# Performance work log

Measured on AMD Instinct MI355X. Metric: run time of the kernel, lower is better.

The kernel has to match this reference:

```python
import jax, jax.numpy as jnp
import numpy as np
import math

N_QUBITS = 8
EMBED_DIM = 8
NUM_HEADS = 2
N_QLAYERS = 2
TWO_PI = 2.0 * math.pi


def _apply_rx(state, theta, wire):
    # state: (N,) + (2,)*n complex64; theta: scalar or (N,)
    n = state.ndim - 1
    ax = 1 + wire
    a0 = jnp.take(state, 0, axis=ax)
    a1 = jnp.take(state, 1, axis=ax)
    half = jnp.asarray(theta) * 0.5
    c = jnp.cos(half)
    s = jnp.sin(half)
    if c.ndim:  # per-sample angle -> broadcast over remaining qubit axes
        bshape = (-1,) + (1,) * (n - 1)
        c = c.reshape(bshape)
        s = s.reshape(bshape)
    js = 1j * s
    n0 = c * a0 - js * a1
    n1 = -js * a0 + c * a1
    return jnp.stack([n0, n1], axis=ax)


def _apply_cnot(state, ctrl, tgt):
    ac, at = 1 + ctrl, 1 + tgt
    s0 = jnp.take(state, 0, axis=ac)
    s1 = jnp.take(state, 1, axis=ac)
    at2 = at - 1 if at > ac else at  # target axis index after removing control axis
    s1 = jnp.flip(s1, axis=at2)
    return jnp.stack([s0, s1], axis=ac)


def qnode(inputs, weights):
    """AngleEmbedding(RX) + BasicEntanglerLayers(RX + CNOT ring), PauliZ expvals.
    inputs: (N, n) angles; weights: (L, n). Returns (N, n) expvals, fully batched."""
    N, n = inputs.shape
    L = weights.shape[0]
    state = jnp.zeros((N,) + (2,) * n, jnp.complex64)
    state = state.at[(slice(None),) + (0,) * n].set(1.0)
    for i in range(n):  # AngleEmbedding: RX(inputs[:, i]) on wire i
        state = _apply_rx(state, inputs[:, i], i)
    for l in range(L):  # BasicEntanglerLayers
        for i in range(n):
            state = _apply_rx(state, weights[l, i], i)
        for i in range(n):
            state = _apply_cnot(state, i, (i + 1) % n)
    probs = (state.real ** 2 + state.imag ** 2).reshape(N, 2 ** n)
    # wire 0 is the most significant bit of the flattened statevector index
    idx = jnp.arange(2 ** n)
    bits = (idx[:, None] >> jnp.arange(n - 1, -1, -1)[None, :]) & 1  # (2^n, n)
    signs = (1.0 - 2.0 * bits).astype(probs.dtype)
    return probs @ signs  # (N, n)


def _qproj(x, weights):
    # apply qnode to every (batch, timestep) vector at once (vectorized loop fusion)
    B, S, E = x.shape
    return qnode(x.reshape(B * S, E), weights).reshape(B, S, E)


def _attention_forward(q, k, v, wq_w, wk_w, wv_w, wd_w):
    B, S, E = q.shape
    H, D = NUM_HEADS, EMBED_DIM // NUM_HEADS
    qp = _qproj(q, wq_w)
    kp = _qproj(k, wk_w)
    vp = _qproj(v, wv_w)
    # split heads: (B, H, S, D)
    qh = qp.reshape(B, S, H, D).transpose(0, 2, 1, 3)
    kh = kp.reshape(B, S, H, D).transpose(0, 2, 1, 3)
    vh = vp.reshape(B, S, H, D).transpose(0, 2, 1, 3)
    scores = jnp.einsum('bhqd,bhkd->bhqk', qh, kh) / jnp.sqrt(jnp.asarray(D, qh.dtype))
    attn = jax.nn.softmax(scores, axis=-1)
    ctx = jnp.einsum('bhqk,bhkd->bhqd', attn, vh)
    concat = ctx.transpose(0, 2, 1, 3).reshape(B, S, E)
    out = _qproj(concat, wd_w)
    return out, attn


def setup_inputs() -> dict:
    key = jax.random.key(0)
    kq, kk, kv, k1, k2, k3, k4 = jax.random.split(key, 7)
    B, S, E = 32, 1024, EMBED_DIM
    return {
        'q': jax.random.normal(kq, (B, S, E), jnp.float32),
        'k': jax.random.normal(kk, (B, S, E), jnp.float32),
        'v': jax.random.normal(kv, (B, S, E), jnp.float32),
        'wq_weights': jax.random.uniform(k1, (N_QLAYERS, N_QUBITS), jnp.float32) * TWO_PI,
        'wk_weights': jax.random.uniform(k2, (N_QLAYERS, N_QUBITS), jnp.float32) * TWO_PI,
        'wv_weights': jax.random.uniform(k3, (N_QLAYERS, N_QUBITS), jnp.float32) * TWO_PI,
        'dense_weights': jax.random.uniform(k4, (N_QLAYERS, N_QUBITS), jnp.float32) * TWO_PI,
    }


def reference(q, k, v, wq_weights, wk_weights, wv_weights, dense_weights):
    return _attention_forward(q, k, v, wq_weights, wk_weights, wv_weights, dense_weights)
```

## Files before the change

### kernel.cpp

```cpp
#include <hip/hip_runtime.h>
#include <math.h>


#define NSAMP 32768

#define QX1 0xB1
#define QX2 0x4E
#define QX3 0x1B
#define ROW_MIRROR 0x140
#define ROW_HALF_MIRROR 0x141

template <int CTRL>
__device__ __forceinline__ float dppf(float x) {
  int xi = __float_as_int(x);
  return __int_as_float(
      __builtin_amdgcn_update_dpp(xi, xi, CTRL, 0xF, 0xF, false));
}

template <int P1>
__device__ __forceinline__ float dpp2x(float x) {
  return dppf<ROW_HALF_MIRROR>(dppf<P1>(x));
}


template <int CTRL>
__device__ __forceinline__ void cg1(float c, float s, float* vr, float* vi) {
#pragma unroll
  for (int m = 0; m < 32; ++m) {
    const float pr = dppf<CTRL>(vr[m]);
    const float pi = dppf<CTRL>(vi[m]);
    vr[m] = fmaf(c, vr[m], s * pi);
    vi[m] = fmaf(c, vi[m], -s * pr);
  }
}

template <int P1>
__device__ __forceinline__ void cg2(float c, float s, float* vr, float* vi) {
#pragma unroll
  for (int m = 0; m < 32; ++m) {
    const float pr = dpp2x<P1>(vr[m]);
    const float pi = dpp2x<P1>(vi[m]);
    vr[m] = fmaf(c, vr[m], s * pi);
    vi[m] = fmaf(c, vi[m], -s * pr);
  }
}

template <int P1, bool TWO, int ML>
__device__ __forceinline__ void cgl(float c, float s, float* vr, float* vi) {
  constexpr int HB = ML >= 16 ? 16 : ML >= 8 ? 8 : ML >= 4 ? 4
                     : ML >= 2 ? 2 : 1;
#pragma unroll
  for (int m = 0; m < 32; ++m) {
    if (!(m & HB)) {
      const int p = m ^ ML;
      float prl, pil, prp, pip;
      if constexpr (TWO) {
        prl = dpp2x<P1>(vr[p]); pil = dpp2x<P1>(vi[p]);
        prp = dpp2x<P1>(vr[m]); pip = dpp2x<P1>(vi[m]);
      } else {
        prl = dppf<P1>(vr[p]); pil = dppf<P1>(vi[p]);
        prp = dppf<P1>(vr[m]); pip = dppf<P1>(vi[m]);
      }
      vr[m] = fmaf(c, vr[m], s * pil);
      vi[m] = fmaf(c, vi[m], -s * prl);
      vr[p] = fmaf(c, vr[p], s * pip);
      vi[p] = fmaf(c, vi[p], -s * prp);
    }
  }
}

template <int ML>
__device__ __forceinline__ void gl(float c, float s, float* vr, float* vi) {
  constexpr int HB = ML >= 16 ? 16 : ML >= 8 ? 8 : ML >= 4 ? 4
                     : ML >= 2 ? 2 : 1;
#pragma unroll
  for (int m = 0; m < 32; ++m) {
    if (!(m & HB)) {
      const int p = m ^ ML;
      float a0r = vr[m], a0i = vi[m], a1r = vr[p], a1i = vi[p];
      vr[m] = fmaf(c, a0r, s * a1i);
      vi[m] = fmaf(c, a0i, -s * a1r);
      vr[p] = fmaf(c, a1r, s * a0i);
      vi[p] = fmaf(c, a1i, -s * a0r);
    }
  }
}

__device__ __forceinline__ float lane_wht8(float v, int l3) {
  float u = dppf<QX1>(v);
  v = (l3 & 1) ? (u - v) : (v + u);
  u = dppf<QX2>(v);
  v = (l3 & 2) ? (u - v) : (v + u);
  u = dpp2x<QX3>(v);
  v = (l3 & 4) ? (u - v) : (v + u);
  return v;
}

__device__ __forceinline__ void qsim_wave(const float* __restrict__ in,
                                          float* __restrict__ outp,
                                          int sampBase,
                                          const float* __restrict__ wc,
                                          const float* __restrict__ wsn) {
  const int lane = threadIdx.x & 63;
  const int l3 = lane & 7;
  const int samp = sampBase + (lane >> 3);

  const float* row = in + (size_t)samp * 8;
  float ci[8], si[8];
#pragma unroll
  for (int w = 0; w < 8; ++w) {
    const float half = 0.5f * row[w];
    ci[w] = cosf(half);
    si[w] = sinf(half);
  }

  float mm[32];
  mm[0] = ((l3 & 4) ? si[0] : ci[0]) * ((l3 & 2) ? si[1] : ci[1]) *
          ((l3 & 1) ? si[2] : ci[2]);
#pragma unroll
  for (int k = 0; k < 5; ++k) {
    const float cc = ci[7 - k], ss = si[7 - k];
#pragma unroll
    for (int t = (1 << k) - 1; t >= 0; --t) {
      mm[t + (1 << k)] = mm[t] * ss;
      mm[t] = mm[t] * cc;
    }
  }

  float vr[32], vi[32];
  const int pq = __builtin_popcount(l3) & 3;
#pragma unroll
  for (int m = 0; m < 32; ++m) {
    const int pl = __builtin_popcount(m) & 3;
    const float t = mm[m];
    if (pl == 0) { vr[m] = t;    vi[m] = 0.0f; }
    else if (pl == 1) { vr[m] = 0.0f; vi[m] = -t; }
    else if (pl == 2) { vr[m] = -t;   vi[m] = 0.0f; }
    else { vr[m] = 0.0f; vi[m] = t; }
  }
  if (pq == 1) {
#pragma unroll
    for (int m = 0; m < 32; ++m) {
      const float t = vr[m];
      vr[m] = vi[m];
      vi[m] = -t;
    }
  } else if (pq == 2) {
#pragma unroll
    for (int m = 0; m < 32; ++m) {
      vr[m] = -vr[m];
      vi[m] = -vi[m];
    }
  } else if (pq == 3) {
#pragma unroll
    for (int m = 0; m < 32; ++m) {
      const float t = vr[m];
      vr[m] = -vi[m];
      vi[m] = t;
    }
  }

  cg2<QX3>(wc[0], wsn[0], vr, vi);
  cg1<QX2>(wc[1], wsn[1], vr, vi);
  cg1<QX1>(wc[2], wsn[2], vr, vi);
  gl<0x10>(wc[3], wsn[3], vr, vi);
  gl<0x08>(wc[4], wsn[4], vr, vi);
  gl<0x04>(wc[5], wsn[5], vr, vi);
  gl<0x02>(wc[6], wsn[6], vr, vi);
  gl<0x01>(wc[7], wsn[7], vr, vi);
  cg2<QX1>(wc[8], wsn[8], vr, vi);
  cg1<QX3>(wc[9], wsn[9], vr, vi);
  cgl<QX1, false, 0x10>(wc[10], wsn[10], vr, vi);
  gl<0x18>(wc[11], wsn[11], vr, vi);
  gl<0x0C>(wc[12], wsn[12], vr, vi);
  gl<0x06>(wc[13], wsn[13], vr, vi);
  gl<0x03>(wc[14], wsn[14], vr, vi);
  cgl<QX1, true, 0x01>(wc[15], wsn[15], vr, vi);

  float accA, accB, accC, accD, accE, accF;
#pragma unroll
  for (int g = 0; g < 4; ++g) {
    float w[8];
#pragma unroll
    for (int j = 0; j < 8; ++j) {
      const int m = g * 8 + j;
      w[j] = fmaf(vr[m], vr[m], vi[m] * vi[m]);
    }
#pragma unroll
    for (int k = 0; k < 3; ++k) {
#pragma unroll
      for (int j = 0; j < 8; ++j) {
        if (!(j & (1 << k))) {
          const int j2 = j | (1 << k);
          const float a = w[j], b = w[j2];
          w[j] = a + b;
          w[j2] = a - b;
        }
      }
    }
    if (g == 0) {
      accA = w[5]; accB = w[7]; accC = w[7]; accD = w[7];
      accE = w[3]; accF = w[2];
    } else if (g == 1) {
      accA += w[5]; accB -= w[7]; accC -= w[7]; accD += w[7];
      accE -= w[3]; accF -= w[2];
    } else if (g == 2) {
      accA -= w[5]; accB -= w[7]; accC += w[7]; accD -= w[7];
      accE += w[3]; accF += w[2];
    } else {
      accA -= w[5]; accB += w[7]; accC -= w[7]; accD -= w[7];
      accE -= w[3]; accF -= w[2];
    }
  }

  const float oA = lane_wht8(accA, l3);
  const float oB = lane_wht8(accB, l3);
  const float oC = lane_wht8(accC, l3);
  const float oD = lane_wht8(accD, l3);
  const float oE = lane_wht8(accE, l3);
  const float oF = lane_wht8(accF, l3);

  float* orow = outp + (size_t)samp * 8;
  if (l3 == 6) orow[0] = oA;
  if (l3 == 2) {
    orow[2] = oB;
    orow[4] = oD;
    orow[6] = oA;
  }
  if (l3 == 5) {
    orow[1] = oB;
    orow[3] = oC;
    orow[5] = oE;
    orow[7] = oF;
  }
}

__device__ __forceinline__ void weight_trig(const float* __restrict__ w,
                                            float* __restrict__ tc,
                                            float* __restrict__ tsn) {
  if (threadIdx.x < 32) {
    const int a = threadIdx.x & 15;
    const float half = 0.5f * w[a];
    if (threadIdx.x < 16)
      tc[a] = cosf(half);
    else
      tsn[a] = sinf(half);
  }
  __syncthreads();
}

__global__ __launch_bounds__(256, 4) void mhaq_qproj3_kernel(
    const float* __restrict__ q, const float* __restrict__ k,
    const float* __restrict__ v, const float* __restrict__ wq,
    const float* __restrict__ wk, const float* __restrict__ wv,
    float* __restrict__ qp, float* __restrict__ kp, float* __restrict__ vp) {
  __shared__ float tc[16], tsn[16];
  const int wg = blockIdx.x * 4 + (threadIdx.x >> 6);
  const int proj = wg >> 12;
  const float* wsel = proj == 0 ? wq : proj == 1 ? wk : wv;
  weight_trig(wsel, tc, tsn);
  const float* in = proj == 0 ? q : proj == 1 ? k : v;
  float* op = proj == 0 ? qp : proj == 1 ? kp : vp;
  qsim_wave(in, op, (wg & 4095) * 8, tc, tsn);
}

__global__ __launch_bounds__(256, 4) void mhaq_qproj1_kernel(
    const float* __restrict__ ctx, const float* __restrict__ wd,
    float* __restrict__ outp) {
  __shared__ float tc[16], tsn[16];
  weight_trig(wd, tc, tsn);
  const int wg = blockIdx.x * 4 + (threadIdx.x >> 6);
  qsim_wave(ctx, outp, wg * 8, tc, tsn);
}

__device__ __forceinline__ float wred_sum(float v) {
  v += dppf<QX1>(v);
  v += dppf<QX2>(v);
  v += dppf<ROW_HALF_MIRROR>(v);
  v += dppf<ROW_MIRROR>(v);
  v += __shfl_xor(v, 16, 64);
  v += __shfl_xor(v, 32, 64);
  return v;
}
__device__ __forceinline__ float wred_max(float v) {
  v = fmaxf(v, dppf<QX1>(v));
  v = fmaxf(v, dppf<QX2>(v));
  v = fmaxf(v, dppf<ROW_HALF_MIRROR>(v));
  v = fmaxf(v, dppf<ROW_MIRROR>(v));
  v = fmaxf(v, __shfl_xor(v, 16, 64));
  v = fmaxf(v, __shfl_xor(v, 32, 64));
  return v;
}

__global__ __launch_bounds__(256, 2) void mhaq_attn_kernel(
    const float* __restrict__ qp, const float* __restrict__ kp,
    const float* __restrict__ vp, float* __restrict__ ctx,
    float* __restrict__ attn) {
  const int wg = blockIdx.x * 4 + (threadIdx.x >> 6);
  const int bh = wg >> 7;
  const int chunk = wg & 127;
  const int b = bh >> 1, h = bh & 1;
  const int lane = threadIdx.x & 63;

  float4 kreg[16], vreg[16];
  const float* kbase = kp + (size_t)b * 1024 * 8 + h * 4;
  const float* vbase = vp + (size_t)b * 1024 * 8 + h * 4;
#pragma unroll
  for (int t = 0; t < 4; ++t) {
#pragma unroll
    for (int c = 0; c < 4; ++c) {
      const size_t j = (size_t)t * 256 + lane * 4 + c;
      kreg[t * 4 + c] = *(const float4*)(kbase + j * 8);
      vreg[t * 4 + c] = *(const float4*)(vbase + j * 8);
    }
  }

  for (int r = 0; r < 8; ++r) {
    const int i = chunk * 8 + r;
    const float4 qv = *(const float4*)(qp + ((size_t)b * 1024 + i) * 8 + h * 4);
    float e[16];
    float mx = -1e30f;
#pragma unroll
    for (int t = 0; t < 16; ++t) {
      float s = qv.x * kreg[t].x + qv.y * kreg[t].y + qv.z * kreg[t].z +
                qv.w * kreg[t].w;
      s *= 0.5f;
      e[t] = s;
      mx = fmaxf(mx, s);
    }
    mx = wred_max(mx);
    float sum = 0.0f;
#pragma unroll
    for (int t = 0; t < 16; ++t) {
      e[t] = __expf(e[t] - mx);
      sum += e[t];
    }
    sum = wred_sum(sum);
    const float rinv = 1.0f / sum;

    float a0 = 0.f, a1 = 0.f, a2 = 0.f, a3 = 0.f;
    float* arow = attn + ((size_t)(bh * 1024 + i)) * 1024;
#pragma unroll
    for (int t = 0; t < 4; ++t) {
      float p0 = e[4 * t] * rinv, p1 = e[4 * t + 1] * rinv,
            p2 = e[4 * t + 2] * rinv, p3 = e[4 * t + 3] * rinv;
      *(float4*)(arow + t * 256 + lane * 4) = make_float4(p0, p1, p2, p3);
      a0 = fmaf(p0, vreg[4 * t].x, a0);
      a1 = fmaf(p0, vreg[4 * t].y, a1);
      a2 = fmaf(p0, vreg[4 * t].z, a2);
      a3 = fmaf(p0, vreg[4 * t].w, a3);
      a0 = fmaf(p1, vreg[4 * t + 1].x, a0);
      a1 = fmaf(p1, vreg[4 * t + 1].y, a1);
      a2 = fmaf(p1, vreg[4 * t + 1].z, a2);
      a3 = fmaf(p1, vreg[4 * t + 1].w, a3);
      a0 = fmaf(p2, vreg[4 * t + 2].x, a0);
      a1 = fmaf(p2, vreg[4 * t + 2].y, a1);
      a2 = fmaf(p2, vreg[4 * t + 2].z, a2);
      a3 = fmaf(p2, vreg[4 * t + 2].w, a3);
      a0 = fmaf(p3, vreg[4 * t + 3].x, a0);
      a1 = fmaf(p3, vreg[4 * t + 3].y, a1);
      a2 = fmaf(p3, vreg[4 * t + 3].z, a2);
      a3 = fmaf(p3, vreg[4 * t + 3].w, a3);
    }
    a0 = wred_sum(a0);
    a1 = wred_sum(a1);
    a2 = wred_sum(a2);
    a3 = wred_sum(a3);
    if (lane == 0)
      *(float4*)(ctx + ((size_t)b * 1024 + i) * 8 + h * 4) =
          make_float4(a0, a1, a2, a3);
  }
}

extern "C" void kernel_launch(void* const* d_in, const int* in_sizes, int n_in,
                              void* d_out, int out_size, void* d_ws,
                              size_t ws_size, hipStream_t stream) {
  (void)in_sizes; (void)n_in; (void)out_size; (void)ws_size;
  const float* q = (const float*)d_in[0];
  const float* k = (const float*)d_in[1];
  const float* v = (const float*)d_in[2];
  const float* wq = (const float*)d_in[3];
  const float* wk = (const float*)d_in[4];
  const float* wv = (const float*)d_in[5];
  const float* wd = (const float*)d_in[6];
  float* outp = (float*)d_out;
  float* attn = outp + 262144;

  float* wsf = (float*)d_ws;
  float* qp = wsf;
  float* kp = qp + (size_t)NSAMP * 8;
  float* vp = kp + (size_t)NSAMP * 8;
  float* ctx = vp + (size_t)NSAMP * 8;

  hipLaunchKernelGGL(mhaq_qproj3_kernel, dim3(3072), dim3(256), 0, stream, q,
                     k, v, wq, wk, wv, qp, kp, vp);
  hipLaunchKernelGGL(mhaq_attn_kernel, dim3(2048), dim3(256), 0, stream, qp,
                     kp, vp, ctx, attn);
  hipLaunchKernelGGL(mhaq_qproj1_kernel, dim3(1024), dim3(256), 0, stream,
                     ctx, wd, outp);
}
```

Baseline: 408.6 us.

## Fold embedding into first RX layer, drop softmax max, use nontemporal attn stores

On each wire the input-embedding RX and the first weight-layer RX are merged into one RX whose angle is the sum of the two. The state then starts directly from the merged product state, so the eight first-layer gates are removed. Each lane now computes a single cos/sin pair and broadcasts it across its 8-lane group with shuffles, instead of every lane evaluating all 8 pairs. The initial phase assignment is rewritten to be branch-free. In the attention kernel the softmax max-subtraction and its wave reduction are dropped, which relies on the projected values being bounded expvals so the scores stay small. The large attention matrix is written with nontemporal stores to reduce cache pollution.

```diff
diff --git a/kernel.cpp b/kernel.cpp
--- a/kernel.cpp
+++ b/kernel.cpp
@@ -3,6 +3,8 @@
 
 
 #define NSAMP 32768
+
+typedef float f4 __attribute__((ext_vector_type(4)));
 
 #define QX1 0xB1
 #define QX2 0x4E
@@ -25,23 +27,25 @@
 
 template <int CTRL>
 __device__ __forceinline__ void cg1(float c, float s, float* vr, float* vi) {
+  const float ns = -s;
 #pragma unroll
   for (int m = 0; m < 32; ++m) {
     const float pr = dppf<CTRL>(vr[m]);
     const float pi = dppf<CTRL>(vi[m]);
     vr[m] = fmaf(c, vr[m], s * pi);
-    vi[m] = fmaf(c, vi[m], -s * pr);
+    vi[m] = fmaf(c, vi[m], ns * pr);
   }
 }
 
 template <int P1>
 __device__ __forceinline__ void cg2(float c, float s, float* vr, float* vi) {
+  const float ns = -s;
 #pragma unroll
   for (int m = 0; m < 32; ++m) {
     const float pr = dpp2x<P1>(vr[m]);
     const float pi = dpp2x<P1>(vi[m]);
     vr[m] = fmaf(c, vr[m], s * pi);
-    vi[m] = fmaf(c, vi[m], -s * pr);
+    vi[m] = fmaf(c, vi[m], ns * pr);
   }
 }
 
@@ -49,6 +53,7 @@
 __device__ __forceinline__ void cgl(float c, float s, float* vr, float* vi) {
   constexpr int HB = ML >= 16 ? 16 : ML >= 8 ? 8 : ML >= 4 ? 4
                      : ML >= 2 ? 2 : 1;
+  const float ns = -s;
 #pragma unroll
   for (int m = 0; m < 32; ++m) {
     if (!(m & HB)) {
@@ -62,9 +67,9 @@
         prp = dppf<P1>(vr[m]); pip = dppf<P1>(vi[m]);
       }
       vr[m] = fmaf(c, vr[m], s * pil);
-      vi[m] = fmaf(c, vi[m], -s * prl);
+      vi[m] = fmaf(c, vi[m], ns * prl);
       vr[p] = fmaf(c, vr[p], s * pip);
-      vi[p] = fmaf(c, vi[p], -s * prp);
+      vi[p] = fmaf(c, vi[p], ns * prp);
     }
   }
 }
@@ -73,15 +78,16 @@
 __device__ __forceinline__ void gl(float c, float s, float* vr, float* vi) {
   constexpr int HB = ML >= 16 ? 16 : ML >= 8 ? 8 : ML >= 4 ? 4
                      : ML >= 2 ? 2 : 1;
+  const float ns = -s;
 #pragma unroll
   for (int m = 0; m < 32; ++m) {
     if (!(m & HB)) {
       const int p = m ^ ML;
       float a0r = vr[m], a0i = vi[m], a1r = vr[p], a1i = vi[p];
       vr[m] = fmaf(c, a0r, s * a1i);
-      vi[m] = fmaf(c, a0i, -s * a1r);
+      vi[m] = fmaf(c, a0i, ns * a1r);
       vr[p] = fmaf(c, a1r, s * a0i);
-      vi[p] = fmaf(c, a1i, -s * a0r);
+      vi[p] = fmaf(c, a1i, ns * a0r);
     }
   }
 }
@@ -100,18 +106,20 @@
                                           float* __restrict__ outp,
                                           int sampBase,
                                           const float* __restrict__ wc,
-                                          const float* __restrict__ wsn) {
+                                          const float* __restrict__ wsn,
+                                          const float* __restrict__ thw) {
   const int lane = threadIdx.x & 63;
   const int l3 = lane & 7;
   const int samp = sampBase + (lane >> 3);
 
-  const float* row = in + (size_t)samp * 8;
+  const float x = in[(size_t)samp * 8 + l3];
+  const float h = 0.5f * x + thw[l3];
+  const float c = cosf(h), s = sinf(h);
   float ci[8], si[8];
 #pragma unroll
   for (int w = 0; w < 8; ++w) {
-    const float half = 0.5f * row[w];
-    ci[w] = cosf(half);
-    si[w] = sinf(half);
+    ci[w] = __shfl(c, w, 8);
+    si[w] = __shfl(s, w, 8);
   }
 
   float mm[32];
@@ -127,47 +135,21 @@
     }
   }
 
+  const int pq = __builtin_popcount(l3) & 3;
+  const float a = (pq == 0) ? 1.0f : (pq == 2) ? -1.0f : 0.0f;
+  const float b = (pq == 1) ? 1.0f : (pq == 3) ? -1.0f : 0.0f;
+  const float na = -a, nb = -b;
   float vr[32], vi[32];
-  const int pq = __builtin_popcount(l3) & 3;
 #pragma unroll
   for (int m = 0; m < 32; ++m) {
     const int pl = __builtin_popcount(m) & 3;
     const float t = mm[m];
-    if (pl == 0) { vr[m] = t;    vi[m] = 0.0f; }
-    else if (pl == 1) { vr[m] = 0.0f; vi[m] = -t; }
-    else if (pl == 2) { vr[m] = -t;   vi[m] = 0.0f; }
-    else { vr[m] = 0.0f; vi[m] = t; }
-  }
-  if (pq == 1) {
-#pragma unroll
-    for (int m = 0; m < 32; ++m) {
-      const float t = vr[m];
-      vr[m] = vi[m];
-      vi[m] = -t;
-    }
-  } else if (pq == 2) {
-#pragma unroll
-    for (int m = 0; m < 32; ++m) {
-      vr[m] = -vr[m];
-      vi[m] = -vi[m];
-    }
-  } else if (pq == 3) {
-#pragma unroll
-    for (int m = 0; m < 32; ++m) {
-      const float t = vr[m];
-      vr[m] = -vi[m];
-      vi[m] = t;
-    }
-  }
-
-  cg2<QX3>(wc[0], wsn[0], vr, vi);
-  cg1<QX2>(wc[1], wsn[1], vr, vi);
-  cg1<QX1>(wc[2], wsn[2], vr, vi);
-  gl<0x10>(wc[3], wsn[3], vr, vi);
-  gl<0x08>(wc[4], wsn[4], vr, vi);
-  gl<0x04>(wc[5], wsn[5], vr, vi);
-  gl<0x02>(wc[6], wsn[6], vr, vi);
-  gl<0x01>(wc[7], wsn[7], vr, vi);
+    if (pl == 0) { vr[m] = a * t;  vi[m] = nb * t; }
+    else if (pl == 1) { vr[m] = nb * t; vi[m] = na * t; }
+    else if (pl == 2) { vr[m] = na * t; vi[m] = b * t; }
+    else { vr[m] = b * t;  vi[m] = a * t; }
+  }
+
   cg2<QX1>(wc[8], wsn[8], vr, vi);
   cg1<QX3>(wc[9], wsn[9], vr, vi);
   cgl<QX1, false, 0x10>(wc[10], wsn[10], vr, vi);
@@ -192,9 +174,9 @@
       for (int j = 0; j < 8; ++j) {
         if (!(j & (1 << k))) {
           const int j2 = j | (1 << k);
-          const float a = w[j], b = w[j2];
-          w[j] = a + b;
-          w[j2] = a - b;
+          const float p2 = w[j], q2 = w[j2];
+          w[j] = p2 + q2;
+          w[j2] = p2 - q2;
         }
       }
     }
@@ -237,14 +219,17 @@
 
 __device__ __forceinline__ void weight_trig(const float* __restrict__ w,
                                             float* __restrict__ tc,
-                                            float* __restrict__ tsn) {
+                                            float* __restrict__ tsn,
+                                            float* __restrict__ thw) {
   if (threadIdx.x < 32) {
     const int a = threadIdx.x & 15;
     const float half = 0.5f * w[a];
-    if (threadIdx.x < 16)
+    if (threadIdx.x < 16) {
       tc[a] = cosf(half);
-    else
+      if (a < 8) thw[a] = half;
+    } else {
       tsn[a] = sinf(half);
+    }
   }
   __syncthreads();
 }
@@ -254,23 +239,23 @@
     const float* __restrict__ v, const float* __restrict__ wq,
     const float* __restrict__ wk, const float* __restrict__ wv,
     float* __restrict__ qp, float* __restrict__ kp, float* __restrict__ vp) {
-  __shared__ float tc[16], tsn[16];
+  __shared__ float tc[16], tsn[16], thw[8];
   const int wg = blockIdx.x * 4 + (threadIdx.x >> 6);
   const int proj = wg >> 12;
   const float* wsel = proj == 0 ? wq : proj == 1 ? wk : wv;
-  weight_trig(wsel, tc, tsn);
+  weight_trig(wsel, tc, tsn, thw);
   const float* in = proj == 0 ? q : proj == 1 ? k : v;
   float* op = proj == 0 ? qp : proj == 1 ? kp : vp;
-  qsim_wave(in, op, (wg & 4095) * 8, tc, tsn);
+  qsim_wave(in, op, (wg & 4095) * 8, tc, tsn, thw);
 }
 
 __global__ __launch_bounds__(256, 4) void mhaq_qproj1_kernel(
     const float* __restrict__ ctx, const float* __restrict__ wd,
     float* __restrict__ outp) {
-  __shared__ float tc[16], tsn[16];
-  weight_trig(wd, tc, tsn);
+  __shared__ float tc[16], tsn[16], thw[8];
+  weight_trig(wd, tc, tsn, thw);
   const int wg = blockIdx.x * 4 + (threadIdx.x >> 6);
-  qsim_wave(ctx, outp, wg * 8, tc, tsn);
+  qsim_wave(ctx, outp, wg * 8, tc, tsn, thw);
 }
 
 __device__ __forceinline__ float wred_sum(float v) {
@@ -280,15 +265,6 @@
   v += dppf<ROW_MIRROR>(v);
   v += __shfl_xor(v, 16, 64);
   v += __shfl_xor(v, 32, 64);
-  return v;
-}
-__device__ __forceinline__ float wred_max(float v) {
-  v = fmaxf(v, dppf<QX1>(v));
-  v = fmaxf(v, dppf<QX2>(v));
-  v = fmaxf(v, dppf<ROW_HALF_MIRROR>(v));
-  v = fmaxf(v, dppf<ROW_MIRROR>(v));
-  v = fmaxf(v, __shfl_xor(v, 16, 64));
-  v = fmaxf(v, __shfl_xor(v, 32, 64));
   return v;
 }
 
@@ -319,20 +295,12 @@
     const int i = chunk * 8 + r;
     const float4 qv = *(const float4*)(qp + ((size_t)b * 1024 + i) * 8 + h * 4);
     float e[16];
-    float mx = -1e30f;
+    float sum = 0.0f;
 #pragma unroll
     for (int t = 0; t < 16; ++t) {
       float s = qv.x * kreg[t].x + qv.y * kreg[t].y + qv.z * kreg[t].z +
                 qv.w * kreg[t].w;
-      s *= 0.5f;
-      e[t] = s;
-      mx = fmaxf(mx, s);
-    }
-    mx = wred_max(mx);
-    float sum = 0.0f;
-#pragma unroll
-    for (int t = 0; t < 16; ++t) {
-      e[t] = __expf(e[t] - mx);
+      e[t] = __expf(s * 0.5f);
       sum += e[t];
     }
     sum = wred_sum(sum);
@@ -344,7 +312,8 @@
     for (int t = 0; t < 4; ++t) {
       float p0 = e[4 * t] * rinv, p1 = e[4 * t + 1] * rinv,
             p2 = e[4 * t + 2] * rinv, p3 = e[4 * t + 3] * rinv;
-      *(float4*)(arow + t * 256 + lane * 4) = make_float4(p0, p1, p2, p3);
+      f4 pv = {p0, p1, p2, p3};
+      __builtin_nontemporal_store(pv, (f4*)(arow + t * 256 + lane * 4));
       a0 = fmaf(p0, vreg[4 * t].x, a0);
       a1 = fmaf(p0, vreg[4 * t].y, a1);
       a2 = fmaf(p0, vreg[4 * t].z, a2);
```

Measured after the change: 355.1 us. 13.1% less time.
